# Kernel tuning notes

Measured on AMD Instinct MI355X. Metric: run time of the kernel, lower is better.

The kernel has to match this reference:

```python
import jax, jax.numpy as jnp
import numpy as np


def _gen_multi_direction_mask(w, h):
    """Numpy port of MultiDirectionPattern.generate_multi_direction_mask."""
    mask = np.zeros((8, h, w), dtype=np.float32)
    if h % 2 == 0:
        cx, cy = (w - 1) / 2.0, (h - 1) / 2.0
    else:
        cx, cy = w // 2, h // 2
    ii, jj = np.meshgrid(np.arange(w), np.arange(h))  # ii[j,i]=i, jj[j,i]=j
    deg = (np.degrees(np.arctan2(cy - jj, cx - ii)) + 180.0) % 360.0
    for i in range(8):
        d = deg.copy()
        if i == 7:
            d[d == 0] = 360.0
        m = ((d >= i * 45) & (d <= (i + 1) * 45)).astype(np.float32)
        if h % 2 != 0:
            m[int(cy), int(cx)] = 1.0
        mask[i] = m
    return mask


def setup_inputs() -> dict:
    key = jax.random.key(0)
    kx, ks = jax.random.split(key)
    B, C = 256, 2048
    x = jax.random.normal(kx, (B, C, 7, 7), dtype=jnp.float32)
    s = jax.random.uniform(ks, (B, 1, 56, 56), dtype=jnp.float32)
    feat_mask = jnp.asarray(_gen_multi_direction_mask(7, 7))   # [8,7,7]
    sal_mask = _gen_multi_direction_mask(56, 56)               # [8,56,56]
    idx_list = [np.flatnonzero(sal_mask[i].ravel()) for i in range(8)]
    n = idx_list[0].size  # 406; equal for all sectors by symmetry
    assert all(a.size == n for a in idx_list)
    sal_idx = jnp.asarray(np.stack(idx_list).astype(np.int32))  # [8,406]
    return {"x": x, "s": s, "feat_mask": feat_mask, "sal_idx": sal_idx}


def reference(x, s, feat_mask, sal_idx):
    # --- directional mean-pool over the 7x7 feature map ---
    # count of nonzero cells per direction mask, shape [8]
    count = jnp.sum(feat_mask.reshape(8, -1) != 0, axis=-1).astype(x.dtype)
    # (x.unsqueeze(2) * mask).sum(-2).sum(-1) == einsum over hw
    part = jnp.einsum('bchw,phw->bcp', x, feat_mask)   # [B,C,8]
    feat = (part / count).reshape(x.shape[0], x.shape[1], 2, 4)
    # --- directional gather from the 56x56 saliency map ---
    B, Cs = s.shape[0], s.shape[1]
    s_flat = s.reshape(B, Cs, -1)                      # [B,Cs,3136]
    gath = s_flat[:, :, sal_idx]                       # [B,Cs,8,N]
    N = gath.shape[3]
    # torch: per-sector [B, Cs*N] then stack on dim=2 -> [B, Cs*N, 8] -> [B, Cs*N, 2, 4]
    sal_feat = jnp.transpose(gath, (0, 1, 3, 2)).reshape(B, Cs * N, 2, 4)
    return feat, sal_feat
```

## Files before the change

### kernel.cpp

```cpp
#include <hip/hip_runtime.h>


#define KPIX 49
#define TROWS 64
#define TFLOATS (TROWS * KPIX)
#define TF4 (TFLOATS / 4)

__global__ __launch_bounds__(64, 3) void mdp_fused_kernel(
    const float* __restrict__ x, const float* __restrict__ s,
    const float* __restrict__ fm, const int* __restrict__ sidx,
    float* __restrict__ out, int BC, int nb1, int N, int SHW, int qper)
{
    const int lane = threadIdx.x;

    if ((int)blockIdx.x < nb1) {
        __shared__ float xs[TFLOATS];
        const int r0 = blockIdx.x * TROWS;

        float rc[8];
        #pragma unroll
        for (int p = 0; p < 8; ++p) {
            float v = (lane < KPIX) ? fm[p * KPIX + lane] : 0.f;
            unsigned long long bm = __ballot(v != 0.f);
            rc[p] = 1.0f / (float)__popcll(bm);
        }

        const float4* xg = (const float4*)(x + (size_t)r0 * KPIX);
        float4* xs4 = (float4*)xs;
        if (r0 + TROWS <= BC) {
            #pragma unroll
            for (int j = 0; j < 12; ++j) xs4[j * 64 + lane] = xg[j * 64 + lane];
            if (lane < 16) xs4[768 + lane] = xg[768 + lane];
        } else {
            const int nfl = (BC - r0) * KPIX;
            const float* xgs = x + (size_t)r0 * KPIX;
            for (int i = lane; i < nfl; i += 64) xs[i] = xgs[i];
        }
        __syncthreads();

        const int r = r0 + lane;
        if (r < BC) {
            float row[KPIX];
            #pragma unroll
            for (int k = 0; k < KPIX; ++k) row[k] = xs[lane * KPIX + k];

            float sum[8];
            #pragma unroll
            for (int p = 0; p < 8; ++p) {
                float acc = 0.f;
                #pragma unroll
                for (int k = 0; k < KPIX; ++k)
                    acc += row[k] * fm[p * KPIX + k];
                sum[p] = acc * rc[p];
            }
            float4* o = (float4*)(out + (size_t)r * 8);
            o[0] = make_float4(sum[0], sum[1], sum[2], sum[3]);
            o[1] = make_float4(sum[4], sum[5], sum[6], sum[7]);
        }
    } else {
        const int bq = blockIdx.x - nb1;
        const int b = bq / qper, q = bq % qper;
        const int tot = N * 8;
        const int chunk = tot / qper;
        const float* srow = s + (size_t)b * SHW;
        float* o2 = out + (size_t)BC * 8 + (size_t)b * tot + (size_t)q * chunk;
        for (int i = lane; i < chunk; i += 64) {
            const int e = q * chunk + i;
            o2[i] = srow[sidx[(e & 7) * N + (e >> 3)]];
        }
    }
}

extern "C" void kernel_launch(void* const* d_in, const int* in_sizes, int n_in,
                              void* d_out, int out_size, void* d_ws, size_t ws_size,
                              hipStream_t stream) {
    const float* x    = (const float*)d_in[0];
    const float* s    = (const float*)d_in[1];
    const float* fm   = (const float*)d_in[2];
    const int*   sidx = (const int*)d_in[3];
    float* out = (float*)d_out;

    const int SHW = 3136;
    const int B   = in_sizes[1] / SHW;
    const int BC  = in_sizes[0] / KPIX;
    const int N   = in_sizes[3] / 8;

    const int nb1  = (BC + TROWS - 1) / TROWS;
    const int qper = ((N * 8) % 4 == 0) ? 4 : 1;
    const int grid = nb1 + B * qper;

    mdp_fused_kernel<<<grid, 64, 0, stream>>>(x, s, fm, sidx, out,
                                              BC, nb1, N, SHW, qper);
}
```

Before: 166.4 us.

## Drop shared-memory staging; each lane loads four contiguous rows directly via float4

The LDS staging buffer and barrier are removed. Each thread now reads its own 4 rows (196 floats, 49 float4 loads) straight from global memory and accumulates the 8 directional sums in registers, with the row and column for every element resolved at compile time. This avoids the shared-memory round trip and the block sync, and cuts the number of x-blocks by four. In exchange, global loads are strided per lane (uncoalesced across the wavefront), register pressure rises, and there are fewer blocks for the memory-bound pass over x.

```diff
diff --git a/kernel.cpp b/kernel.cpp
--- a/kernel.cpp
+++ b/kernel.cpp
@@ -2,9 +2,8 @@
 
 
 #define KPIX 49
-#define TROWS 64
-#define TFLOATS (TROWS * KPIX)
-#define TF4 (TFLOATS / 4)
+#define RPL 4
+#define RPB (64 * RPL)
 
 __global__ __launch_bounds__(64, 3) void mdp_fused_kernel(
     const float* __restrict__ x, const float* __restrict__ s,
@@ -14,9 +13,6 @@
     const int lane = threadIdx.x;
 
     if ((int)blockIdx.x < nb1) {
-        __shared__ float xs[TFLOATS];
-        const int r0 = blockIdx.x * TROWS;
-
         float rc[8];
         #pragma unroll
         for (int p = 0; p < 8; ++p) {
@@ -25,37 +21,53 @@
             rc[p] = 1.0f / (float)__popcll(bm);
         }
 
-        const float4* xg = (const float4*)(x + (size_t)r0 * KPIX);
-        float4* xs4 = (float4*)xs;
-        if (r0 + TROWS <= BC) {
+        const int r0 = blockIdx.x * RPB + lane * RPL;
+        if (r0 + RPL <= BC) {
+            const float4* base = (const float4*)(x + (size_t)r0 * KPIX);
+            float acc[RPL][8];
             #pragma unroll
-            for (int j = 0; j < 12; ++j) xs4[j * 64 + lane] = xg[j * 64 + lane];
-            if (lane < 16) xs4[768 + lane] = xg[768 + lane];
+            for (int rr = 0; rr < RPL; ++rr)
+                #pragma unroll
+                for (int p = 0; p < 8; ++p) acc[rr][p] = 0.f;
+
+            #pragma unroll
+            for (int j = 0; j < KPIX; ++j) {
+                const float4 v = base[j];
+                #pragma unroll
+                for (int c = 0; c < 4; ++c) {
+                    const int f   = j * 4 + c;
+                    const int row = f / KPIX;
+                    const int col = f % KPIX;
+                    const float e = (c == 0) ? v.x : (c == 1) ? v.y
+                                  : (c == 2) ? v.z : v.w;
+                    #pragma unroll
+                    for (int p = 0; p < 8; ++p)
+                        acc[row][p] += e * fm[p * KPIX + col];
+                }
+            }
+
+            float4* o = (float4*)(out + (size_t)r0 * 8);
+            #pragma unroll
+            for (int rr = 0; rr < RPL; ++rr) {
+                o[rr * 2 + 0] = make_float4(acc[rr][0] * rc[0], acc[rr][1] * rc[1],
+                                            acc[rr][2] * rc[2], acc[rr][3] * rc[3]);
+                o[rr * 2 + 1] = make_float4(acc[rr][4] * rc[4], acc[rr][5] * rc[5],
+                                            acc[rr][6] * rc[6], acc[rr][7] * rc[7]);
+            }
         } else {
-            const int nfl = (BC - r0) * KPIX;
-            const float* xgs = x + (size_t)r0 * KPIX;
-            for (int i = lane; i < nfl; i += 64) xs[i] = xgs[i];
-        }
-        __syncthreads();
-
-        const int r = r0 + lane;
-        if (r < BC) {
-            float row[KPIX];
-            #pragma unroll
-            for (int k = 0; k < KPIX; ++k) row[k] = xs[lane * KPIX + k];
-
-            float sum[8];
-            #pragma unroll
-            for (int p = 0; p < 8; ++p) {
-                float acc = 0.f;
+            for (int rr = 0; rr < RPL; ++rr) {
+                const int r = r0 + rr;
+                if (r >= BC) break;
+                float sum[8];
                 #pragma unroll
-                for (int k = 0; k < KPIX; ++k)
-                    acc += row[k] * fm[p * KPIX + k];
-                sum[p] = acc * rc[p];
+                for (int p = 0; p < 8; ++p) sum[p] = 0.f;
+                for (int k = 0; k < KPIX; ++k) {
+                    const float e = x[(size_t)r * KPIX + k];
+                    #pragma unroll
+                    for (int p = 0; p < 8; ++p) sum[p] += e * fm[p * KPIX + k];
+                }
+                for (int p = 0; p < 8; ++p) out[(size_t)r * 8 + p] = sum[p] * rc[p];
             }
-            float4* o = (float4*)(out + (size_t)r * 8);
-            o[0] = make_float4(sum[0], sum[1], sum[2], sum[3]);
-            o[1] = make_float4(sum[4], sum[5], sum[6], sum[7]);
         }
     } else {
         const int bq = blockIdx.x - nb1;
@@ -85,7 +97,7 @@
     const int BC  = in_sizes[0] / KPIX;
     const int N   = in_sizes[3] / 8;
 
-    const int nb1  = (BC + TROWS - 1) / TROWS;
+    const int nb1  = (BC + RPB - 1) / RPB;
     const int qper = ((N * 8) % 4 == 0) ? 4 : 1;
     const int grid = nb1 + B * qper;
 
```

Measured after the change: 175.7 us. +5.6%, slower.

## Use 256-thread blocks with per-wave tiles and split directions across half-waves

Applied to the files above, without the earlier changes.

Blocks grow to four wavefronts, and each wave owns a 32-row slice of the feature tile in shared memory. Each wave waits on its own loads with a waitcnt instead of a block-wide barrier, since no wave reads another wave's slice. Each lane computes 4 of the 8 directional sums for one row, so both half-waves share the row loads and register pressure drops. The saliency gather blocks also use 256 threads. The aim is more loads in flight and higher occupancy, in exchange for reading each row from LDS twice.

```diff
diff --git a/kernel.cpp b/kernel.cpp
--- a/kernel.cpp
+++ b/kernel.cpp
@@ -2,20 +2,23 @@
 
 
 #define KPIX 49
-#define TROWS 64
-#define TFLOATS (TROWS * KPIX)
-#define TF4 (TFLOATS / 4)
+#define WROWS 32
+#define WFLOATS (WROWS * KPIX)
+#define WF4 (WFLOATS / 4)
+#define BROWS (WROWS * 4)
 
-__global__ __launch_bounds__(64, 3) void mdp_fused_kernel(
+__global__ __launch_bounds__(256, 6) void mdp_feat_sal_kernel(
     const float* __restrict__ x, const float* __restrict__ s,
     const float* __restrict__ fm, const int* __restrict__ sidx,
     float* __restrict__ out, int BC, int nb1, int N, int SHW, int qper)
 {
-    const int lane = threadIdx.x;
+    const int tid  = threadIdx.x;
+    const int wid  = tid >> 6;
+    const int lane = tid & 63;
 
     if ((int)blockIdx.x < nb1) {
-        __shared__ float xs[TFLOATS];
-        const int r0 = blockIdx.x * TROWS;
+        __shared__ float xs[4 * WFLOATS];
+        float* slice = &xs[wid * WFLOATS];
 
         float rc[8];
         #pragma unroll
@@ -25,37 +28,40 @@
             rc[p] = 1.0f / (float)__popcll(bm);
         }
 
-        const float4* xg = (const float4*)(x + (size_t)r0 * KPIX);
-        float4* xs4 = (float4*)xs;
-        if (r0 + TROWS <= BC) {
+        const int w0 = (blockIdx.x * 4 + wid) * WROWS;
+        if (w0 >= BC) return;
+
+        const float4* xg = (const float4*)(x + (size_t)w0 * KPIX);
+        float4* s4 = (float4*)slice;
+        if (w0 + WROWS <= BC) {
             #pragma unroll
-            for (int j = 0; j < 12; ++j) xs4[j * 64 + lane] = xg[j * 64 + lane];
-            if (lane < 16) xs4[768 + lane] = xg[768 + lane];
+            for (int j = 0; j < 6; ++j) s4[j * 64 + lane] = xg[j * 64 + lane];
+            if (lane < WF4 - 384) s4[384 + lane] = xg[384 + lane];
         } else {
-            const int nfl = (BC - r0) * KPIX;
-            const float* xgs = x + (size_t)r0 * KPIX;
-            for (int i = lane; i < nfl; i += 64) xs[i] = xgs[i];
+            const int nfl = (BC - w0) * KPIX;
+            const float* xgs = x + (size_t)w0 * KPIX;
+            for (int i = lane; i < nfl; i += 64) slice[i] = xgs[i];
         }
-        __syncthreads();
+        __builtin_amdgcn_s_waitcnt(0);
 
-        const int r = r0 + lane;
-        if (r < BC) {
-            float row[KPIX];
-            #pragma unroll
-            for (int k = 0; k < KPIX; ++k) row[k] = xs[lane * KPIX + k];
-
-            float sum[8];
-            #pragma unroll
-            for (int p = 0; p < 8; ++p) {
-                float acc = 0.f;
+        {
+            const int rloc = lane & 31;
+            const int r    = w0 + rloc;
+            const int phalf = (lane >> 5) * 4;
+            if (r < BC) {
+                const float* row = &slice[rloc * KPIX];
+                float acc[4] = {0.f, 0.f, 0.f, 0.f};
                 #pragma unroll
-                for (int k = 0; k < KPIX; ++k)
-                    acc += row[k] * fm[p * KPIX + k];
-                sum[p] = acc * rc[p];
+                for (int k = 0; k < KPIX; ++k) {
+                    const float e = row[k];
+                    #pragma unroll
+                    for (int q = 0; q < 4; ++q)
+                        acc[q] += e * fm[(phalf + q) * KPIX + k];
+                }
+                float4* o = (float4*)(out + (size_t)r * 8 + phalf);
+                *o = make_float4(acc[0] * rc[phalf + 0], acc[1] * rc[phalf + 1],
+                                 acc[2] * rc[phalf + 2], acc[3] * rc[phalf + 3]);
             }
-            float4* o = (float4*)(out + (size_t)r * 8);
-            o[0] = make_float4(sum[0], sum[1], sum[2], sum[3]);
-            o[1] = make_float4(sum[4], sum[5], sum[6], sum[7]);
         }
     } else {
         const int bq = blockIdx.x - nb1;
@@ -64,7 +70,7 @@
         const int chunk = tot / qper;
         const float* srow = s + (size_t)b * SHW;
         float* o2 = out + (size_t)BC * 8 + (size_t)b * tot + (size_t)q * chunk;
-        for (int i = lane; i < chunk; i += 64) {
+        for (int i = tid; i < chunk; i += 256) {
             const int e = q * chunk + i;
             o2[i] = srow[sidx[(e & 7) * N + (e >> 3)]];
         }
@@ -85,10 +91,10 @@
     const int BC  = in_sizes[0] / KPIX;
     const int N   = in_sizes[3] / 8;
 
-    const int nb1  = (BC + TROWS - 1) / TROWS;
+    const int nb1  = (BC + BROWS - 1) / BROWS;
     const int qper = ((N * 8) % 4 == 0) ? 4 : 1;
     const int grid = nb1 + B * qper;
 
-    mdp_fused_kernel<<<grid, 64, 0, stream>>>(x, s, fm, sidx, out,
-                                              BC, nb1, N, SHW, qper);
+    mdp_feat_sal_kernel<<<grid, 256, 0, stream>>>(x, s, fm, sidx, out,
+                                                  BC, nb1, N, SHW, qper);
 }
```

Result: slower. 185.0 us (+11.2%).
